# Kernel tuning notes

Hardware: AMD Instinct MI355X
Metric: run time of the kernel (lower is better)

Reference implementation:

```python
import jax, jax.numpy as jnp
import numpy as np

B, C, H, W = 16, 512, 24, 24


def setup_inputs() -> dict:
    key = jax.random.key(0)
    ks = jax.random.split(key, 7)
    s = 0.02
    return {
        "x5": jax.random.normal(ks[0], (B, C, H, W), jnp.float32),
        "conv_w": jax.random.normal(ks[1], (C, C), jnp.float32) * s,
        "conv_b": jax.random.normal(ks[2], (C,), jnp.float32) * s,
        "q_w": jax.random.normal(ks[3], (C, C), jnp.float32) * s,
        "q_b": jax.random.normal(ks[4], (C,), jnp.float32) * s,
        "k_w": jax.random.normal(ks[5], (C, C), jnp.float32) * s,
        "k_b": jax.random.normal(ks[6], (C,), jnp.float32) * s,
    }


def _conv1x1(x, w, b):
    # 1x1 conv == channel matmul: (O,C) x (B,C,H,W) -> (B,O,H,W)
    return jnp.einsum('oc,bchw->bohw', w, x) + b[None, :, None, None]


def reference(x5, conv_w, conv_b, q_w, q_b, k_w, k_b):
    Bb, Cc, Hh, Ww = x5.shape
    scale = 1.0 / (Cc ** 0.5)
    x5 = _conv1x1(x5, conv_w, conv_b) + x5
    # my_SS2D source was not provided in the module; treated as identity (see notes)
    x00 = x5
    # cross-batch correlation: queries (B*H*W, C), keys (B, C, H*W)
    q = _conv1x1(x00, q_w, q_b).reshape(Bb, Cc, Hh * Ww).transpose(0, 2, 1).reshape(Bb * Hh * Ww, Cc)
    k = _conv1x1(x00, k_w, k_b).reshape(Bb, Cc, Hh * Ww)
    # scores: (B*H*W, B, H*W); max over locations, mean over images
    scores = jnp.einsum('nc,bcm->nbm', q, k) * scale
    x_w = scores.max(axis=-1).mean(axis=-1).reshape(Bb, Hh * Ww)
    x_w = jax.nn.softmax(x_w, axis=-1)
    # channel-wise L2 normalize (F.normalize, eps=1e-12)
    nrm = jnp.sqrt(jnp.sum(x5 * x5, axis=1, keepdims=True))
    norm0 = x5 / jnp.maximum(nrm, 1e-12)
    # top-1 (equality-based) seed mask per image
    x_w_max = x_w.max(axis=-1, keepdims=True)
    mask = (x_w == x_w_max).astype(x5.dtype).reshape(Bb, 1, Hh, Ww)
    seeds = (norm0 * mask).sum(axis=(2, 3))  # (B, C)
    # seeded 1x1-conv correlation (eval mode -> relu): (B, B_seeds, H, W)
    corr = jax.nn.relu(jnp.einsum('bchw,sc->bshw', norm0, seeds)).mean(axis=1).reshape(Bb, Hh * Ww)
    mn = corr.min(axis=-1, keepdims=True)
    mx = corr.max(axis=-1, keepdims=True)
    cormap = ((corr - mn) / (mx - mn + 1e-12)).reshape(Bb, 1, Hh, Ww)
    x51 = x5 * cormap
    proto1 = jnp.mean(x51, axis=(0, 2, 3), keepdims=True)  # (1, C, 1, 1)
    return (x5, proto1, x5 * proto1 + x51, mask)
```

## Files before the change

kernel.cpp:

```cpp
#include <hip/hip_runtime.h>
#include <math.h>

#define BB   16
#define CC   512
#define HWW  576
#define NN   9216
#define CHW  (CC*HWW)
#define TOT  (BB*CHW)
#define SCALE 0.044194173824159216f
#define FRAGB 9437184

typedef __attribute__((ext_vector_type(8))) __bf16 bf16x8;
typedef __attribute__((ext_vector_type(4))) float f32x4;


__global__ __launch_bounds__(256)
void prep_x_kernel(const float* __restrict__ X, __bf16* __restrict__ Xhi,
                   __bf16* __restrict__ Xlo)
{
    int g = blockIdx.x * 256 + threadIdx.x;
    int n = g % NN;
    int co = g / NN;
    int c0 = co * 8;
    int bimg = n / HWW, mm = n % HWW;
    const float* src = X + (size_t)bimg * CHW + mm;
    union { __bf16 h[8]; float4 f4; } uh, ul;
#pragma unroll
    for (int j = 0; j < 8; j++) {
        float v = src[(size_t)(c0 + j) * HWW];
        __bf16 h = (__bf16)v;
        uh.h[j] = h;
        ul.h[j] = (__bf16)(v - (float)h);
    }
    int Cb = c0 >> 6, s = (c0 >> 5) & 1, q8 = (c0 >> 3) & 3;
    int T = n >> 6, g4 = (n >> 4) & 3, Lm = n & 15;
    size_t off = (size_t)(Cb * 144 + T) * 4096 + (s * 4 + g4) * 512 + (size_t)((q8 << 4) | Lm) * 8;
    *(float4*)&Xhi[off] = uh.f4;
    *(float4*)&Xlo[off] = ul.f4;
}

__global__ __launch_bounds__(256)
void prep_w_kernel(const float* __restrict__ cw, const float* __restrict__ qw,
                   const float* __restrict__ kw, __bf16* __restrict__ cwhi,
                   __bf16* __restrict__ cwlo, __bf16* __restrict__ qwf,
                   __bf16* __restrict__ kwf)
{
    int y = blockIdx.y;
    const float* W = (y == 0) ? cw : (y == 1) ? qw : kw;
    __bf16* dh = (y == 0) ? cwhi : (y == 1) ? qwf : kwf;
    int g = blockIdx.x * 256 + threadIdx.x;
    int o = g >> 6;
    int c0 = (g & 63) * 8;
    union { __bf16 h[8]; float4 f4; } uh, ul;
#pragma unroll
    for (int j = 0; j < 8; j++) {
        float v = W[(size_t)o * CC + c0 + j];
        __bf16 h = (__bf16)v;
        uh.h[j] = h;
        ul.h[j] = (__bf16)(v - (float)h);
    }
    int Cb = c0 >> 6, s = (c0 >> 5) & 1, q8 = (c0 >> 3) & 3;
    int To = o >> 6, g4 = (o >> 4) & 3, Lm = o & 15;
    size_t off = (size_t)(Cb * 8 + To) * 4096 + (s * 4 + g4) * 512 + (size_t)((q8 << 4) | Lm) * 8;
    *(float4*)&dh[off] = uh.f4;
    if (y == 0) *(float4*)&cwlo[off] = ul.f4;
}

__global__ __launch_bounds__(256)
void conv1_mfma_kernel(const float* __restrict__ X, const __bf16* __restrict__ Whi,
                       const __bf16* __restrict__ Wlo, const __bf16* __restrict__ Xhi,
                       const __bf16* __restrict__ Xlo, const float* __restrict__ bias,
                       float* __restrict__ Y, __bf16* __restrict__ Yfrag)
{
    __shared__ __bf16 lAh[8192], lAl[8192], lBh[8192], lBl[8192];
    int tid = threadIdx.x, lane = tid & 63, wv = tid >> 6;
    int wo = wv >> 1, wm = wv & 1;
    int m0 = blockIdx.x * 128;
    int o0 = blockIdx.y * 128;
    int oT0 = blockIdx.y * 2, mT0 = blockIdx.x * 2;

    f32x4 acc[4][4];
#pragma unroll
    for (int i = 0; i < 4; i++)
#pragma unroll
        for (int j = 0; j < 4; j++) acc[i][j] = (f32x4){0.f, 0.f, 0.f, 0.f};

    for (int Cb = 0; Cb < 8; Cb++) {
        const float4* gAh = (const float4*)(Whi + (size_t)(Cb * 8 + oT0) * 4096);
        const float4* gAl = (const float4*)(Wlo + (size_t)(Cb * 8 + oT0) * 4096);
        const float4* gBh = (const float4*)(Xhi + (size_t)(Cb * 144 + mT0) * 4096);
        const float4* gBl = (const float4*)(Xlo + (size_t)(Cb * 144 + mT0) * 4096);
        float4* dAh = (float4*)lAh; float4* dAl = (float4*)lAl;
        float4* dBh = (float4*)lBh; float4* dBl = (float4*)lBl;
#pragma unroll
        for (int i = 0; i < 4; i++) {
            dAh[tid + i * 256] = gAh[tid + i * 256];
            dAl[tid + i * 256] = gAl[tid + i * 256];
            dBh[tid + i * 256] = gBh[tid + i * 256];
            dBl[tid + i * 256] = gBl[tid + i * 256];
        }
        __syncthreads();
#pragma unroll
        for (int s = 0; s < 2; s++) {
            bf16x8 ah[4], al[4], bh[4], bl[4];
#pragma unroll
            for (int ga = 0; ga < 4; ga++) {
                ah[ga] = *(const bf16x8*)&lAh[wo * 4096 + (s * 4 + ga) * 512 + lane * 8];
                al[ga] = *(const bf16x8*)&lAl[wo * 4096 + (s * 4 + ga) * 512 + lane * 8];
            }
#pragma unroll
            for (int gb = 0; gb < 4; gb++) {
                bh[gb] = *(const bf16x8*)&lBh[wm * 4096 + (s * 4 + gb) * 512 + lane * 8];
                bl[gb] = *(const bf16x8*)&lBl[wm * 4096 + (s * 4 + gb) * 512 + lane * 8];
            }
#pragma unroll
            for (int ga = 0; ga < 4; ga++)
#pragma unroll
                for (int gb = 0; gb < 4; gb++) {
                    acc[ga][gb] = __builtin_amdgcn_mfma_f32_16x16x32_bf16(ah[ga], bh[gb], acc[ga][gb], 0, 0, 0);
                    acc[ga][gb] = __builtin_amdgcn_mfma_f32_16x16x32_bf16(ah[ga], bl[gb], acc[ga][gb], 0, 0, 0);
                    acc[ga][gb] = __builtin_amdgcn_mfma_f32_16x16x32_bf16(al[ga], bh[gb], acc[ga][gb], 0, 0, 0);
                }
        }
        __syncthreads();
    }

    int quad = lane >> 4, col = lane & 15;
#pragma unroll
    for (int ga = 0; ga < 4; ga++) {
        int ob = o0 + wo * 64 + ga * 16 + quad * 4;
        float bs[4];
#pragma unroll
        for (int r = 0; r < 4; r++) bs[r] = bias[ob + r];
        int Cb2 = ob >> 6, s2 = (ob >> 5) & 1, q8 = (ob >> 3) & 3, j0 = ob & 7;
#pragma unroll
        for (int gb = 0; gb < 4; gb++) {
            int n = m0 + wm * 64 + gb * 16 + col;
            int T = n >> 6, g4 = (n >> 4) & 3, Lm = n & 15;
            int bimg = n / HWW, mm = n % HWW;
            size_t xb = (size_t)bimg * CHW + mm;
            union { __bf16 h[4]; float2 f2; } u;
#pragma unroll
            for (int r = 0; r < 4; r++) {
                float v = acc[ga][gb][r] + bs[r] + X[xb + (size_t)(ob + r) * HWW];
                Y[xb + (size_t)(ob + r) * HWW] = v;
                u.h[r] = (__bf16)v;
            }
            *(float2*)&Yfrag[(size_t)(Cb2 * 144 + T) * 4096 + (s2 * 4 + g4) * 512 + (size_t)((q8 << 4) | Lm) * 8 + j0] = u.f2;
        }
    }
}

__global__ __launch_bounds__(256)
void convqk_mfma_kernel(const __bf16* __restrict__ qwf, const __bf16* __restrict__ kwf,
                        const float* __restrict__ qb, const float* __restrict__ kb,
                        const __bf16* __restrict__ Xf, __bf16* __restrict__ Oq,
                        __bf16* __restrict__ Ok)
{
    const __bf16* Wf = blockIdx.z ? kwf : qwf;
    const float* bias = blockIdx.z ? kb : qb;
    __bf16* Of = blockIdx.z ? Ok : Oq;

    __shared__ __bf16 lA[8192], lB[8192];
    int tid = threadIdx.x, lane = tid & 63, wv = tid >> 6;
    int wo = wv >> 1, wm = wv & 1;
    int m0 = blockIdx.x * 128;
    int o0 = blockIdx.y * 128;
    int oT0 = blockIdx.y * 2, mT0 = blockIdx.x * 2;

    f32x4 acc[4][4];
#pragma unroll
    for (int i = 0; i < 4; i++)
#pragma unroll
        for (int j = 0; j < 4; j++) acc[i][j] = (f32x4){0.f, 0.f, 0.f, 0.f};

    for (int Cb = 0; Cb < 8; Cb++) {
        const float4* gA = (const float4*)(Wf + (size_t)(Cb * 8 + oT0) * 4096);
        const float4* gB = (const float4*)(Xf + (size_t)(Cb * 144 + mT0) * 4096);
        float4* dA = (float4*)lA; float4* dB = (float4*)lB;
#pragma unroll
        for (int i = 0; i < 4; i++) {
            dA[tid + i * 256] = gA[tid + i * 256];
            dB[tid + i * 256] = gB[tid + i * 256];
        }
        __syncthreads();
#pragma unroll
        for (int s = 0; s < 2; s++) {
            bf16x8 af[4], bf[4];
#pragma unroll
            for (int ga = 0; ga < 4; ga++)
                af[ga] = *(const bf16x8*)&lA[wo * 4096 + (s * 4 + ga) * 512 + lane * 8];
#pragma unroll
            for (int gb = 0; gb < 4; gb++)
                bf[gb] = *(const bf16x8*)&lB[wm * 4096 + (s * 4 + gb) * 512 + lane * 8];
#pragma unroll
            for (int ga = 0; ga < 4; ga++)
#pragma unroll
                for (int gb = 0; gb < 4; gb++)
                    acc[ga][gb] = __builtin_amdgcn_mfma_f32_16x16x32_bf16(af[ga], bf[gb], acc[ga][gb], 0, 0, 0);
        }
        __syncthreads();
    }

    int quad = lane >> 4, col = lane & 15;
#pragma unroll
    for (int ga = 0; ga < 4; ga++) {
        int ob = o0 + wo * 64 + ga * 16 + quad * 4;
        float bs[4];
#pragma unroll
        for (int r = 0; r < 4; r++) bs[r] = bias[ob + r];
        int Cb2 = ob >> 6, s2 = (ob >> 5) & 1, q8 = (ob >> 3) & 3, j0 = ob & 7;
#pragma unroll
        for (int gb = 0; gb < 4; gb++) {
            int n = m0 + wm * 64 + gb * 16 + col;
            int T = n >> 6, g4 = (n >> 4) & 3, Lm = n & 15;
            union { __bf16 h[4]; float2 f2; } u;
#pragma unroll
            for (int r = 0; r < 4; r++) u.h[r] = (__bf16)(acc[ga][gb][r] + bs[r]);
            *(float2*)&Of[(size_t)(Cb2 * 144 + T) * 4096 + (s2 * 4 + g4) * 512 + (size_t)((q8 << 4) | Lm) * 8 + j0] = u.f2;
        }
    }
}

__global__ __launch_bounds__(256)
void scores_mfma_kernel(const __bf16* __restrict__ Qf, const __bf16* __restrict__ Kf,
                        float* __restrict__ maxv3)
{
    __shared__ __bf16 ldsQ[12288];
    __shared__ __bf16 ldsK[12288];
    __shared__ float redbuf[192][2];

    int tid = threadIdx.x, lane = tid & 63, wv = tid >> 6;
    int wq = wv >> 1, wk = wv & 1;
    int bx = blockIdx.x;
    int n0 = bx * 192;
    int b = blockIdx.y / 3, mt = blockIdx.y % 3;

    f32x4 acc[6][6];
#pragma unroll
    for (int ga = 0; ga < 6; ga++)
#pragma unroll
        for (int t = 0; t < 6; t++) acc[ga][t] = (f32x4){0.f, 0.f, 0.f, 0.f};

    const __bf16* qbase = Qf + (size_t)(bx * 3) * 4096;
    const __bf16* kbase = Kf + (size_t)(b * 9 + mt * 3) * 4096;

    for (int C = 0; C < 8; C++) {
        const float4* gq = (const float4*)(qbase + (size_t)C * 144 * 4096);
        const float4* gk = (const float4*)(kbase + (size_t)C * 144 * 4096);
        float4* lq = (float4*)ldsQ;
        float4* lk = (float4*)ldsK;
#pragma unroll
        for (int i = 0; i < 6; i++) {
            lq[tid + i * 256] = gq[tid + i * 256];
            lk[tid + i * 256] = gk[tid + i * 256];
        }
        __syncthreads();
#pragma unroll
        for (int s = 0; s < 2; s++) {
            bf16x8 af[6], bfr[6];
#pragma unroll
            for (int ga = 0; ga < 6; ga++) {
                int qrow = wq * 96 + ga * 16;
                af[ga] = *(const bf16x8*)&ldsQ[(qrow >> 6) * 4096 + (s * 4 + ((qrow >> 4) & 3)) * 512 + lane * 8];
            }
#pragma unroll
            for (int t = 0; t < 6; t++) {
                int krow = wk * 96 + t * 16;
                bfr[t] = *(const bf16x8*)&ldsK[(krow >> 6) * 4096 + (s * 4 + ((krow >> 4) & 3)) * 512 + lane * 8];
            }
#pragma unroll
            for (int ga = 0; ga < 6; ga++)
#pragma unroll
                for (int t = 0; t < 6; t++)
                    acc[ga][t] = __builtin_amdgcn_mfma_f32_16x16x32_bf16(af[ga], bfr[t], acc[ga][t], 0, 0, 0);
        }
        __syncthreads();
    }

    float mg[6][4];
#pragma unroll
    for (int ga = 0; ga < 6; ga++)
#pragma unroll
        for (int r = 0; r < 4; r++) {
            float v = acc[ga][0][r];
#pragma unroll
            for (int t = 1; t < 6; t++) v = fmaxf(v, acc[ga][t][r]);
            mg[ga][r] = v;
        }
#pragma unroll
    for (int off = 1; off < 16; off <<= 1)
#pragma unroll
        for (int ga = 0; ga < 6; ga++)
#pragma unroll
            for (int r = 0; r < 4; r++)
                mg[ga][r] = fmaxf(mg[ga][r], __shfl_xor(mg[ga][r], off, 64));

    if ((lane & 15) == 0) {
        int quad = lane >> 4;
#pragma unroll
        for (int ga = 0; ga < 6; ga++)
#pragma unroll
            for (int r = 0; r < 4; r++)
                redbuf[wq * 96 + ga * 16 + quad * 4 + r][wk] = mg[ga][r];
    }
    __syncthreads();
    if (tid < 192) {
        float rv = fmaxf(redbuf[tid][0], redbuf[tid][1]) * SCALE;
        maxv3[((size_t)(n0 + tid) * BB + b) * 3 + mt] = rv;
    }
}

__global__ __launch_bounds__(576)
void topk_kernel(const float* __restrict__ maxv3, int* __restrict__ cand)
{
    __shared__ float sv[576];
    __shared__ float rv_[64];
    __shared__ int ri_[64];
    int bi = blockIdx.x, m = threadIdx.x;
    int n = bi * HWW + m;
    float v = 0.f;
#pragma unroll
    for (int t = 0; t < BB; t++) {
        const float* p = maxv3 + ((size_t)n * BB + t) * 3;
        v += fmaxf(fmaxf(p[0], p[1]), p[2]);
    }
    sv[m] = v;
    __syncthreads();
    for (int r = 0; r < 4; r++) {
        if (m < 64) {
            float bv = sv[m]; int bidx = m;
            for (int j = m + 64; j < 576; j += 64)
                if (sv[j] > bv) { bv = sv[j]; bidx = j; }
            rv_[m] = bv; ri_[m] = bidx;
        }
        __syncthreads();
        if (m == 0) {
            float bv = rv_[0]; int bidx = ri_[0];
            for (int j = 1; j < 64; j++)
                if (rv_[j] > bv) { bv = rv_[j]; bidx = ri_[j]; }
            cand[bi * 4 + r] = bidx;
            sv[bidx] = -3.4e38f;
        }
        __syncthreads();
    }
}

__global__ __launch_bounds__(256)
void refine_q_kernel(const float* __restrict__ x5, const float* __restrict__ qw,
                     const float* __restrict__ qb, const int* __restrict__ cand,
                     float* __restrict__ q_all)
{
    int og = blockIdx.x, cd = blockIdx.y;
    int bi = cd >> 2;
    int mstar = cand[cd];
    int tid = threadIdx.x, w = tid >> 6, lane = tid & 63;
    __shared__ float xcol[512];
    __shared__ float qrows[64];
    xcol[tid]       = x5[(size_t)bi * CHW + tid * HWW + mstar];
    xcol[tid + 256] = x5[(size_t)bi * CHW + (tid + 256) * HWW + mstar];
    __syncthreads();
#pragma unroll
    for (int i = 0; i < 16; i++) {
        int r = og * 64 + w * 16 + i;
        float p = 0.f;
#pragma unroll
        for (int it = 0; it < 8; it++) {
            int c = lane + it * 64;
            p = fmaf(qw[(size_t)r * 512 + c], xcol[c], p);
        }
        for (int off = 32; off; off >>= 1) p += __shfl_down(p, off, 64);
        if (lane == 0) qrows[w * 16 + i] = p;
    }
    __syncthreads();
    if (tid < 64) q_all[(size_t)cd * 512 + og * 64 + tid] = qrows[tid] + qb[og * 64 + tid];
}

__global__ __launch_bounds__(256)
void refine_u2_kernel(const float* __restrict__ kw, const float* __restrict__ kb,
                      const float* __restrict__ q_all, float* __restrict__ u_all,
                      float* __restrict__ qkbg)
{
    int tg = blockIdx.x, cd = blockIdx.y;
    int tid = threadIdx.x;
    __shared__ float qs[512];
    qs[tid]       = q_all[(size_t)cd * 512 + tid];
    qs[tid + 256] = q_all[(size_t)cd * 512 + tid + 256];
    __syncthreads();
    int t = tg * 256 + tid;
    float u = 0.f;
    for (int o = 0; o < 512; o++)
        u = fmaf(kw[(size_t)o * 512 + t], qs[o], u);
    u_all[(size_t)cd * 512 + t] = u;
    if (tg == 0) {
        float pk = qs[tid] * kb[tid] + qs[tid + 256] * kb[tid + 256];
        for (int off = 32; off; off >>= 1) pk += __shfl_down(pk, off, 64);
        __shared__ float pr[4];
        if ((tid & 63) == 0) pr[tid >> 6] = pk;
        __syncthreads();
        if (tid == 0) qkbg[cd] = pr[0] + pr[1] + pr[2] + pr[3];
    }
}

__global__ __launch_bounds__(256)
void refine_max_kernel(const float* __restrict__ x5, const float* __restrict__ u_all,
                       float* __restrict__ maxex9)
{
    int bp = blockIdx.x, cg = blockIdx.y, mc = blockIdx.z;
    int tid = threadIdx.x, mi = tid & 63, cs = tid >> 6;
    int m0 = mc * 64;
    __shared__ float us[16 * 512];
    __shared__ float red[256];
    for (int e = tid; e < 16 * 512; e += 256) us[e] = u_all[(size_t)cg * 16 * 512 + e];
    __syncthreads();

    float acc[16];
#pragma unroll
    for (int j = 0; j < 16; j++) acc[j] = 0.f;
    const float* xb = x5 + (size_t)bp * CHW + m0 + mi;
    for (int cc = 0; cc < 128; cc++) {
        int c = cs * 128 + cc;
        float x = xb[(size_t)c * HWW];
#pragma unroll
        for (int j = 0; j < 16; j++)
            acc[j] = fmaf(us[j * 512 + c], x, acc[j]);
    }

#pragma unroll
    for (int j = 0; j < 16; j++) {
        red[tid] = acc[j];
        __syncthreads();
        if (tid < 64) {
            float v = red[tid] + red[tid + 64] + red[tid + 128] + red[tid + 192];
            for (int off = 32; off; off >>= 1) v = fmaxf(v, __shfl_xor(v, off, 64));
            if (tid == 0) maxex9[((size_t)(cg * 16 + j) * BB + bp) * 9 + mc] = v;
        }
        __syncthreads();
    }
}

__global__ __launch_bounds__(576)
void mask_kernel(const float* __restrict__ maxex9, const float* __restrict__ qkbg,
                 const int* __restrict__ cand, float* __restrict__ maskout)
{
    int bi = blockIdx.x, m = threadIdx.x;
    __shared__ float ve[4];
    __shared__ int chosen;
    if (m < 4) {
        int cd = bi * 4 + m;
        float sacc = 0.f;
#pragma unroll
        for (int t = 0; t < BB; t++) {
            const float* p = maxex9 + ((size_t)cd * BB + t) * 9;
            float mv = p[0];
#pragma unroll
            for (int z = 1; z < 9; z++) mv = fmaxf(mv, p[z]);
            sacc += mv;
        }
        ve[m] = sacc * (1.f / 16.f) + qkbg[cd];
    }
    __syncthreads();
    if (m == 0) {
        int best = 0; float bv = ve[0];
        for (int j = 1; j < 4; j++) if (ve[j] > bv) { bv = ve[j]; best = j; }
        chosen = cand[bi * 4 + best];
    }
    __syncthreads();
    maskout[bi * HWW + m] = (m == chosen) ? 1.f : 0.f;
}

__global__ __launch_bounds__(256)
void norm_kernel(const float* __restrict__ X5, float* __restrict__ invb)
{
    int b = blockIdx.y;
    int m0 = blockIdx.x * 64;
    int mi = threadIdx.x & 63, cs = threadIdx.x >> 6;
    float s = 0.f;
    for (int c = cs; c < CC; c += 4) {
        float x = X5[b * CHW + c * HWW + m0 + mi];
        s = fmaf(x, x, s);
    }
    __shared__ float red[4][64];
    red[cs][mi] = s;
    __syncthreads();
    if (cs == 0) {
        float t = red[0][mi] + red[1][mi] + red[2][mi] + red[3][mi];
        invb[b * HWW + m0 + mi] = 1.0f / fmaxf(sqrtf(t), 1e-12f);
    }
}

__global__ __launch_bounds__(256)
void seeds_kernel(const float* __restrict__ X5, const float* __restrict__ invb,
                  const float* __restrict__ maskf, float* __restrict__ seeds)
{
    int s = blockIdx.y;
    int c = blockIdx.x * 4 + (threadIdx.x >> 6);
    int mi = threadIdx.x & 63;
    float acc = 0.f;
    for (int mt = 0; mt < 9; mt++) {
        int m = mt * 64 + mi;
        float w = invb[s * HWW + m] * maskf[s * HWW + m];
        acc = fmaf(X5[s * CHW + c * HWW + m], w, acc);
    }
    for (int off = 32; off > 0; off >>= 1) acc += __shfl_down(acc, off, 64);
    if (mi == 0) seeds[s * CC + c] = acc;
}

__global__ __launch_bounds__(256)
void corr_kernel(const float* __restrict__ X5, const float* __restrict__ invb,
                 const float* __restrict__ seeds, float* __restrict__ corr)
{
    __shared__ float sd[16 * 512];
    __shared__ float xs[64][65];
    __shared__ float red[4][64];
    int b = blockIdx.y;
    int m0 = blockIdx.x * 64;
    int tid = threadIdx.x;
    int mi = tid & 63, sg = tid >> 6;

    for (int e = tid; e < 16 * 512; e += 256) sd[e] = seeds[e];

    float acc[4] = {0.f, 0.f, 0.f, 0.f};
    for (int c0 = 0; c0 < CC; c0 += 64) {
        __syncthreads();
        for (int e = tid; e < 4096; e += 256) {
            int mm = e & 63, kk = e >> 6;
            xs[kk][mm] = X5[b * CHW + (c0 + kk) * HWW + m0 + mm];
        }
        __syncthreads();
#pragma unroll
        for (int kk = 0; kk < 64; kk++) {
            float xv = xs[kk][mi];
#pragma unroll
            for (int t = 0; t < 4; t++)
                acc[t] = fmaf(xv, sd[(sg * 4 + t) * CC + c0 + kk], acc[t]);
        }
    }
    float r = 0.f;
#pragma unroll
    for (int t = 0; t < 4; t++) r += fmaxf(acc[t], 0.f);
    red[sg][mi] = r;
    __syncthreads();
    if (sg == 0) {
        float tot = red[0][mi] + red[1][mi] + red[2][mi] + red[3][mi];
        corr[b * HWW + m0 + mi] = invb[b * HWW + m0 + mi] * tot * (1.0f / 16.0f);
    }
}

__global__ __launch_bounds__(576)
void cormap_kernel(const float* __restrict__ corr, float* __restrict__ cormap)
{
    __shared__ float sv[576];
    __shared__ float smn[64], smx[64];
    __shared__ float s_mn, s_mx;
    int b = blockIdx.x;
    int m = threadIdx.x;
    float v = corr[b * HWW + m];
    sv[m] = v;
    __syncthreads();
    if (m < 64) {
        float mn = sv[m], mx = sv[m];
        for (int j = m + 64; j < 576; j += 64) { mn = fminf(mn, sv[j]); mx = fmaxf(mx, sv[j]); }
        smn[m] = mn; smx[m] = mx;
    }
    __syncthreads();
    if (m == 0) {
        float mn = smn[0], mx = smx[0];
        for (int j = 1; j < 64; j++) { mn = fminf(mn, smn[j]); mx = fmaxf(mx, smx[j]); }
        s_mn = mn; s_mx = mx;
    }
    __syncthreads();
    cormap[b * HWW + m] = (v - s_mn) / (s_mx - s_mn + 1e-12f);
}

__global__ __launch_bounds__(256)
void proto_kernel(const float* __restrict__ X5, const float* __restrict__ cormap,
                  float* __restrict__ proto1)
{
    int c = blockIdx.x;
    int tid = threadIdx.x;
    float acc = 0.f;
    for (int p = tid; p < NN; p += 256) {
        int b = p / HWW, m = p % HWW;
        acc = fmaf(X5[b * CHW + c * HWW + m], cormap[p], acc);
    }
    for (int off = 32; off > 0; off >>= 1) acc += __shfl_down(acc, off, 64);
    __shared__ float red[4];
    if ((tid & 63) == 0) red[tid >> 6] = acc;
    __syncthreads();
    if (tid == 0) proto1[c] = (red[0] + red[1] + red[2] + red[3]) * (1.0f / (float)NN);
}

__global__ __launch_bounds__(256)
void final_kernel(const float* __restrict__ X5, const float* __restrict__ proto1,
                  const float* __restrict__ cormap, float* __restrict__ out3)
{
    int idx = blockIdx.x * 256 + threadIdx.x;
    if (idx >= TOT) return;
    int b = idx / CHW;
    int r = idx % CHW;
    int c = r / HWW;
    int m = r % HWW;
    float x = X5[idx];
    out3[idx] = x * (proto1[c] + cormap[b * HWW + m]);
}

extern "C" void kernel_launch(void* const* d_in, const int* in_sizes, int n_in,
                              void* d_out, int out_size, void* d_ws, size_t ws_size,
                              hipStream_t stream)
{
    const float* x  = (const float*)d_in[0];
    const float* cw = (const float*)d_in[1];
    const float* cb = (const float*)d_in[2];
    const float* qw = (const float*)d_in[3];
    const float* qb = (const float*)d_in[4];
    const float* kw = (const float*)d_in[5];
    const float* kb = (const float*)d_in[6];

    float* out     = (float*)d_out;
    float* x5o     = out;
    float* proto1  = out + TOT;
    float* out3    = out + TOT + 512;
    float* maskout = out + TOT + 512 + TOT;

    char* o3 = (char*)out3;
    __bf16* xlo    = (__bf16*)o3;
    __bf16* qfrag  = (__bf16*)o3;
    __bf16* x5frag = (__bf16*)(o3 + FRAGB);

    char* ws = (char*)d_ws;
    __bf16* xhi   = (__bf16*)ws;
    __bf16* kfrag = (__bf16*)ws;
    __bf16* cwhi  = (__bf16*)(ws + FRAGB);
    __bf16* cwlo  = (__bf16*)(ws + FRAGB + 524288);
    __bf16* qwf   = (__bf16*)(ws + FRAGB + 2 * 524288);
    __bf16* kwf   = (__bf16*)(ws + FRAGB + 3 * 524288);
    char* p = ws + FRAGB + 4 * 524288;
    float* maxv3  = (float*)p;   p += (size_t)NN * BB * 3 * 4;
    int*   cand   = (int*)p;     p += 256;
    float* q_all  = (float*)p;   p += 64 * 512 * 4;
    float* u_all  = (float*)p;   p += 64 * 512 * 4;
    float* qkbg   = (float*)p;   p += 256;
    float* maxex9 = (float*)p;   p += 64 * BB * 9 * 4;
    float* invb   = (float*)p;   p += NN * 4;
    float* corr   = (float*)p;   p += NN * 4;
    float* cmap   = (float*)p;   p += NN * 4;
    float* seeds  = (float*)p;   p += BB * CC * 4;

    prep_x_kernel<<<NN * 64 / 256, 256, 0, stream>>>(x, xhi, xlo);
    prep_w_kernel<<<dim3(128, 3), 256, 0, stream>>>(cw, qw, kw, cwhi, cwlo, qwf, kwf);

    conv1_mfma_kernel<<<dim3(NN / 128, 4), 256, 0, stream>>>(x, cwhi, cwlo, xhi, xlo, cb, x5o, x5frag);
    convqk_mfma_kernel<<<dim3(NN / 128, 4, 2), 256, 0, stream>>>(qwf, kwf, qb, kb, x5frag, qfrag, kfrag);

    scores_mfma_kernel<<<dim3(NN / 192, BB * 3), 256, 0, stream>>>(qfrag, kfrag, maxv3);

    topk_kernel<<<BB, HWW, 0, stream>>>(maxv3, cand);
    refine_q_kernel<<<dim3(8, 64), 256, 0, stream>>>(x5o, qw, qb, cand, q_all);
    refine_u2_kernel<<<dim3(2, 64), 256, 0, stream>>>(kw, kb, q_all, u_all, qkbg);
    refine_max_kernel<<<dim3(BB, 4, 9), 256, 0, stream>>>(x5o, u_all, maxex9);
    mask_kernel<<<BB, HWW, 0, stream>>>(maxex9, qkbg, cand, maskout);

    norm_kernel<<<dim3(9, BB), 256, 0, stream>>>(x5o, invb);
    seeds_kernel<<<dim3(CC / 4, BB), 256, 0, stream>>>(x5o, invb, maskout, seeds);
    corr_kernel<<<dim3(9, BB), 256, 0, stream>>>(x5o, invb, seeds, corr);
    cormap_kernel<<<BB, HWW, 0, stream>>>(corr, cmap);
    proto_kernel<<<CC, 256, 0, stream>>>(x5o, cmap, proto1);
    final_kernel<<<(TOT + 255) / 256, 256, 0, stream>>>(x5o, proto1, cmap, out3);
}
```

Measured before the change: 420.4 us.

## Use direct global-to-LDS loads and shrink scores query tile to 128

Replaces the register-staged global-to-shared copies in the conv1, convqk and scores GEMM kernels with the global_load_lds builtin, so tiles go straight into LDS without passing through VGPRs. The scores kernel's query tile drops from 192 to 128 rows, with a 4x6 accumulator per wave, and its reduction buffer now reuses the Q tile's LDS. The aim is lower register pressure and LDS footprint for better occupancy, and more blocks for load balance. The cost is more K-tile reloads per query and reliance on the direct-to-LDS layout matching the old per-thread copy order.

```diff
diff --git a/kernel.cpp b/kernel.cpp
--- a/kernel.cpp
+++ b/kernel.cpp
@@ -13,6 +13,14 @@
 typedef __attribute__((ext_vector_type(8))) __bf16 bf16x8;
 typedef __attribute__((ext_vector_type(4))) float f32x4;
 
+#define AS1 __attribute__((address_space(1)))
+#define AS3 __attribute__((address_space(3)))
+
+static __device__ __forceinline__ void gload_lds16(const void* g, void* l)
+{
+    __builtin_amdgcn_global_load_lds((AS1 const void*)g, (AS3 void*)l, 16, 0, 0);
+}
+
 
 __global__ __launch_bounds__(256)
 void prep_x_kernel(const float* __restrict__ X, __bf16* __restrict__ Xhi,
@@ -90,14 +98,13 @@
         const float4* gAl = (const float4*)(Wlo + (size_t)(Cb * 8 + oT0) * 4096);
         const float4* gBh = (const float4*)(Xhi + (size_t)(Cb * 144 + mT0) * 4096);
         const float4* gBl = (const float4*)(Xlo + (size_t)(Cb * 144 + mT0) * 4096);
-        float4* dAh = (float4*)lAh; float4* dAl = (float4*)lAl;
-        float4* dBh = (float4*)lBh; float4* dBl = (float4*)lBl;
 #pragma unroll
         for (int i = 0; i < 4; i++) {
-            dAh[tid + i * 256] = gAh[tid + i * 256];
-            dAl[tid + i * 256] = gAl[tid + i * 256];
-            dBh[tid + i * 256] = gBh[tid + i * 256];
-            dBl[tid + i * 256] = gBl[tid + i * 256];
+            int eb = wv * 256 + i * 64;
+            gload_lds16(gAh + eb + lane, (float4*)lAh + eb);
+            gload_lds16(gAl + eb + lane, (float4*)lAl + eb);
+            gload_lds16(gBh + eb + lane, (float4*)lBh + eb);
+            gload_lds16(gBl + eb + lane, (float4*)lBl + eb);
         }
         __syncthreads();
 #pragma unroll
@@ -177,11 +184,11 @@
     for (int Cb = 0; Cb < 8; Cb++) {
         const float4* gA = (const float4*)(Wf + (size_t)(Cb * 8 + oT0) * 4096);
         const float4* gB = (const float4*)(Xf + (size_t)(Cb * 144 + mT0) * 4096);
-        float4* dA = (float4*)lA; float4* dB = (float4*)lB;
 #pragma unroll
         for (int i = 0; i < 4; i++) {
-            dA[tid + i * 256] = gA[tid + i * 256];
-            dB[tid + i * 256] = gB[tid + i * 256];
+            int eb = wv * 256 + i * 64;
+            gload_lds16(gA + eb + lane, (float4*)lA + eb);
+            gload_lds16(gB + eb + lane, (float4*)lB + eb);
         }
         __syncthreads();
 #pragma unroll
@@ -226,61 +233,59 @@
 void scores_mfma_kernel(const __bf16* __restrict__ Qf, const __bf16* __restrict__ Kf,
                         float* __restrict__ maxv3)
 {
-    __shared__ __bf16 ldsQ[12288];
+    __shared__ __bf16 ldsQ[8192];
     __shared__ __bf16 ldsK[12288];
-    __shared__ float redbuf[192][2];
 
     int tid = threadIdx.x, lane = tid & 63, wv = tid >> 6;
     int wq = wv >> 1, wk = wv & 1;
     int bx = blockIdx.x;
-    int n0 = bx * 192;
+    int n0 = bx * 128;
     int b = blockIdx.y / 3, mt = blockIdx.y % 3;
 
-    f32x4 acc[6][6];
-#pragma unroll
-    for (int ga = 0; ga < 6; ga++)
+    f32x4 acc[4][6];
+#pragma unroll
+    for (int ga = 0; ga < 4; ga++)
 #pragma unroll
         for (int t = 0; t < 6; t++) acc[ga][t] = (f32x4){0.f, 0.f, 0.f, 0.f};
 
-    const __bf16* qbase = Qf + (size_t)(bx * 3) * 4096;
+    const __bf16* qbase = Qf + (size_t)(bx * 2) * 4096;
     const __bf16* kbase = Kf + (size_t)(b * 9 + mt * 3) * 4096;
 
     for (int C = 0; C < 8; C++) {
         const float4* gq = (const float4*)(qbase + (size_t)C * 144 * 4096);
         const float4* gk = (const float4*)(kbase + (size_t)C * 144 * 4096);
-        float4* lq = (float4*)ldsQ;
-        float4* lk = (float4*)ldsK;
+#pragma unroll
+        for (int i = 0; i < 4; i++) {
+            int eb = wv * 256 + i * 64;
+            gload_lds16(gq + eb + lane, (float4*)ldsQ + eb);
+        }
 #pragma unroll
         for (int i = 0; i < 6; i++) {
-            lq[tid + i * 256] = gq[tid + i * 256];
-            lk[tid + i * 256] = gk[tid + i * 256];
+            int eb = wv * 384 + i * 64;
+            gload_lds16(gk + eb + lane, (float4*)ldsK + eb);
         }
         __syncthreads();
 #pragma unroll
         for (int s = 0; s < 2; s++) {
-            bf16x8 af[6], bfr[6];
-#pragma unroll
-            for (int ga = 0; ga < 6; ga++) {
-                int qrow = wq * 96 + ga * 16;
-                af[ga] = *(const bf16x8*)&ldsQ[(qrow >> 6) * 4096 + (s * 4 + ((qrow >> 4) & 3)) * 512 + lane * 8];
+            bf16x8 af[4];
+#pragma unroll
+            for (int ga = 0; ga < 4; ga++)
+                af[ga] = *(const bf16x8*)&ldsQ[wq * 4096 + (s * 4 + ga) * 512 + lane * 8];
+#pragma unroll
+            for (int t = 0; t < 6; t++) {
+                int mkl = wk * 96 + t * 16;
+                bf16x8 bfr = *(const bf16x8*)&ldsK[(mkl >> 6) * 4096 + (s * 4 + ((mkl >> 4) & 3)) * 512 + lane * 8];
+#pragma unroll
+                for (int ga = 0; ga < 4; ga++)
+                    acc[ga][t] = __builtin_amdgcn_mfma_f32_16x16x32_bf16(af[ga], bfr, acc[ga][t], 0, 0, 0);
             }
-#pragma unroll
-            for (int t = 0; t < 6; t++) {
-                int krow = wk * 96 + t * 16;
-                bfr[t] = *(const bf16x8*)&ldsK[(krow >> 6) * 4096 + (s * 4 + ((krow >> 4) & 3)) * 512 + lane * 8];
-            }
-#pragma unroll
-            for (int ga = 0; ga < 6; ga++)
-#pragma unroll
-                for (int t = 0; t < 6; t++)
-                    acc[ga][t] = __builtin_amdgcn_mfma_f32_16x16x32_bf16(af[ga], bfr[t], acc[ga][t], 0, 0, 0);
-        }
-        __syncthreads();
-    }
-
-    float mg[6][4];
-#pragma unroll
-    for (int ga = 0; ga < 6; ga++)
+        }
+        __syncthreads();
+    }
+
+    float mg[4][4];
+#pragma unroll
+    for (int ga = 0; ga < 4; ga++)
 #pragma unroll
         for (int r = 0; r < 4; r++) {
             float v = acc[ga][0][r];
@@ -291,21 +296,22 @@
 #pragma unroll
     for (int off = 1; off < 16; off <<= 1)
 #pragma unroll
-        for (int ga = 0; ga < 6; ga++)
+        for (int ga = 0; ga < 4; ga++)
 #pragma unroll
             for (int r = 0; r < 4; r++)
                 mg[ga][r] = fmaxf(mg[ga][r], __shfl_xor(mg[ga][r], off, 64));
 
+    float (*redbuf)[2] = (float (*)[2])ldsQ;
     if ((lane & 15) == 0) {
         int quad = lane >> 4;
 #pragma unroll
-        for (int ga = 0; ga < 6; ga++)
+        for (int ga = 0; ga < 4; ga++)
 #pragma unroll
             for (int r = 0; r < 4; r++)
-                redbuf[wq * 96 + ga * 16 + quad * 4 + r][wk] = mg[ga][r];
-    }
-    __syncthreads();
-    if (tid < 192) {
+                redbuf[wq * 64 + ga * 16 + quad * 4 + r][wk] = mg[ga][r];
+    }
+    __syncthreads();
+    if (tid < 128) {
         float rv = fmaxf(redbuf[tid][0], redbuf[tid][1]) * SCALE;
         maxv3[((size_t)(n0 + tid) * BB + b) * 3 + mt] = rv;
     }
@@ -653,7 +659,7 @@
     conv1_mfma_kernel<<<dim3(NN / 128, 4), 256, 0, stream>>>(x, cwhi, cwlo, xhi, xlo, cb, x5o, x5frag);
     convqk_mfma_kernel<<<dim3(NN / 128, 4, 2), 256, 0, stream>>>(qwf, kwf, qb, kb, x5frag, qfrag, kfrag);
 
-    scores_mfma_kernel<<<dim3(NN / 192, BB * 3), 256, 0, stream>>>(qfrag, kfrag, maxv3);
+    scores_mfma_kernel<<<dim3(NN / 128, BB * 3), 256, 0, stream>>>(qfrag, kfrag, maxv3);
 
     topk_kernel<<<BB, HWW, 0, stream>>>(maxv3, cand);
     refine_q_kernel<<<dim3(8, 64), 256, 0, stream>>>(x5o, qw, qb, cand, q_all);
```

Result: faster. 376.6 us (-10.4%).
